# Kernel tuning notes

Hardware: AMD Instinct MI355X
Metric: run time of the kernel (lower is better)

The kernel has to match this reference:

```python
import jax, jax.numpy as jnp
import numpy as np

NUM_NODES = 100000
NUM_EDGES = 600000
NUM_GRAPHS = 512
D = 128  # num_features == latent widths


def setup_inputs() -> dict:
    key = jax.random.key(0)
    ks = jax.random.split(key, 16)
    inp = {
        "x": jax.random.normal(ks[0], (NUM_NODES, D), dtype=jnp.float32),
        "edge_index": jax.random.randint(ks[1], (2, NUM_EDGES), 0, NUM_NODES, dtype=jnp.int32),
        "batch": jnp.sort(jax.random.randint(ks[2], (NUM_NODES,), 0, NUM_GRAPHS, dtype=jnp.int32)),
    }
    s = 1.0 / np.sqrt(D)
    # SAGEConv params per layer: lin_l (applied to mean-aggregated neighbors), lin_r (root), bias
    for i in range(3):
        inp[f"Wl{i+1}"] = jax.random.uniform(ks[3 + 3 * i], (D, D), jnp.float32, -s, s)
        inp[f"Wr{i+1}"] = jax.random.uniform(ks[4 + 3 * i], (D, D), jnp.float32, -s, s)
        inp[f"b{i+1}"] = jax.random.uniform(ks[5 + 3 * i], (D,), jnp.float32, -s, s)
    inp["Wro"] = jax.random.uniform(ks[12], (D, 1), jnp.float32, -s, s)
    inp["bro"] = jax.random.uniform(ks[13], (1,), jnp.float32, -s, s)
    return inp


def _sage_conv(h, Wl, Wr, b, src, dst):
    # mean aggregation of source features at destination nodes
    msg = jax.ops.segment_sum(h[src], dst, num_segments=NUM_NODES)          # [N, D]
    cnt = jax.ops.segment_sum(jnp.ones((src.shape[0], 1), h.dtype), dst,
                              num_segments=NUM_NODES)                        # [N, 1]
    mean = msg / jnp.maximum(cnt, 1.0)
    return mean @ Wl + h @ Wr + b


def reference(x, edge_index, batch, Wl1, Wr1, b1, Wl2, Wr2, b2, Wl3, Wr3, b3, Wro, bro):
    src, dst = edge_index[0], edge_index[1]
    h = x
    for Wl, Wr, b in ((Wl1, Wr1, b1), (Wl2, Wr2, b2), (Wl3, Wr3, b3)):
        h = jax.nn.relu(_sage_conv(h, Wl, Wr, b, src, dst))
    # per-graph sum pooling (replaces the python loop over unique batch ids)
    pooled = jax.ops.segment_sum(h, batch, num_segments=NUM_GRAPHS)  # [G, D]
    return jax.nn.sigmoid(pooled @ Wro + bro)  # [G, 1]
```

## Files before the change

kernel.cpp:

```cpp
#include <hip/hip_runtime.h>
#include <math.h>

#define N_NODES 100000
#define N_EDGES 600000
#define N_GRAPHS 512
#define D 128
#define SCAN_BS 1024
#define SCAN_NBC ((N_NODES + SCAN_BS - 1) / SCAN_BS)
#define NPART 8
#define PART_SZ (N_NODES / NPART)
#define E4 (N_EDGES / 4)
#define SPLIT_B 12500
#define DBINS 64
#define DNB ((N_NODES + 255) / 256)

typedef unsigned short u16;
typedef __attribute__((ext_vector_type(8))) short short8;
typedef __attribute__((ext_vector_type(4))) float f32x4;

__device__ __forceinline__ u16 f2bf(float f) {
    unsigned int u = __float_as_uint(f);
    u += 0x7FFFu + ((u >> 16) & 1u);
    return (u16)(u >> 16);
}
__device__ __forceinline__ float bf2f(u16 h) {
    return __uint_as_float(((unsigned int)h) << 16);
}
__device__ __forceinline__ void split2(float f, unsigned int& h16, unsigned int& l16) {
    unsigned int u = __float_as_uint(f);
    unsigned int hb = (u + (0x7FFFu + ((u >> 16) & 1u))) & 0xffff0000u;
    float lo = f - __uint_as_float(hb);
    unsigned int ul = __float_as_uint(lo);
    h16 = hb >> 16;
    l16 = (ul + (0x7FFFu + ((ul >> 16) & 1u))) >> 16;
}

typedef __attribute__((address_space(1))) const unsigned int gas_u32;
typedef __attribute__((address_space(3))) unsigned int las_u32;
__device__ __forceinline__ void gload16(const void* g, void* l) {
    __builtin_amdgcn_global_load_lds((gas_u32*)g, (las_u32*)l, 16, 0, 0);
}

__global__ __launch_bounds__(256) void zero_i_kernel(int* __restrict__ p, int n) {
    int i = blockIdx.x * 256 + threadIdx.x;
    if (i < n) p[i] = 0;
}

__global__ __launch_bounds__(256) void hist_kernel(const int* __restrict__ dst,
                                                   int* __restrict__ deg) {
    int e = blockIdx.x * 256 + threadIdx.x;
    if (e < N_EDGES) atomicAdd(&deg[dst[e]], 1);
}

__global__ __launch_bounds__(1024) void scan1_kernel(const int* __restrict__ deg,
                                                     int* __restrict__ excl,
                                                     int* __restrict__ blocksum) {
    __shared__ int buf[2][SCAN_BS];
    const int t = threadIdx.x;
    const int gid = blockIdx.x * SCAN_BS + t;
    int v = (gid < N_NODES) ? deg[gid] : 0;
    buf[0][t] = v;
    __syncthreads();
    int pi = 0;
    for (int off = 1; off < SCAN_BS; off <<= 1) {
        int val = buf[pi][t];
        if (t >= off) val += buf[pi][t - off];
        buf[pi ^ 1][t] = val;
        pi ^= 1;
        __syncthreads();
    }
    int incl = buf[pi][t];
    if (gid < N_NODES) excl[gid] = incl - v;
    if (t == SCAN_BS - 1) blocksum[blockIdx.x] = incl;
}

__global__ __launch_bounds__(256) void scan3_kernel(const int* __restrict__ excl,
                                                    const int* __restrict__ blocksum,
                                                    int* __restrict__ rowptr) {
    __shared__ int buf[2][128];
    const int t = threadIdx.x;
    if (t < 128) buf[0][t] = (t < SCAN_NBC) ? blocksum[t] : 0;
    __syncthreads();
    int pi = 0;
    for (int off = 1; off < 128; off <<= 1) {
        if (t < 128) {
            int val = buf[pi][t];
            if (t >= off) val += buf[pi][t - off];
            buf[pi ^ 1][t] = val;
        }
        pi ^= 1;
        __syncthreads();
    }
    const int i = blockIdx.x * 256 + t;
    if (i < N_NODES) {
        const int j = i / SCAN_BS;
        const int pref = (j == 0) ? 0 : buf[pi][j - 1];
        rowptr[i] = excl[i] + pref;
    }
    if (i == 0) rowptr[N_NODES] = N_EDGES;
}

__global__ __launch_bounds__(256) void fill_kernel(const int* __restrict__ src,
                                                   const int* __restrict__ dst,
                                                   const int* __restrict__ rowptr,
                                                   int* __restrict__ fill,
                                                   int* __restrict__ csr_src) {
    const int lo = (blockIdx.x & (NPART - 1)) * PART_SZ;
    const int i4 = (blockIdx.x >> 3) * 256 + threadIdx.x;
    if (i4 >= E4) return;
    const int4 d4 = ((const int4*)dst)[i4];
    const int4 s4 = ((const int4*)src)[i4];
    if ((unsigned)(d4.x - lo) < (unsigned)PART_SZ) {
        int pos = rowptr[d4.x] + atomicAdd(&fill[d4.x], 1);
        csr_src[pos] = s4.x;
    }
    if ((unsigned)(d4.y - lo) < (unsigned)PART_SZ) {
        int pos = rowptr[d4.y] + atomicAdd(&fill[d4.y], 1);
        csr_src[pos] = s4.y;
    }
    if ((unsigned)(d4.z - lo) < (unsigned)PART_SZ) {
        int pos = rowptr[d4.z] + atomicAdd(&fill[d4.z], 1);
        csr_src[pos] = s4.z;
    }
    if ((unsigned)(d4.w - lo) < (unsigned)PART_SZ) {
        int pos = rowptr[d4.w] + atomicAdd(&fill[d4.w], 1);
        csr_src[pos] = s4.w;
    }
}

__global__ __launch_bounds__(256) void dhist_kernel(const int* __restrict__ deg,
                                                    int* __restrict__ histT,
                                                    int* __restrict__ bintot) {
    __shared__ int h[DBINS];
    const int t = threadIdx.x;
    if (t < DBINS) h[t] = 0;
    __syncthreads();
    const int i = blockIdx.x * 256 + t;
    if (i < N_NODES) {
        const int b = 63 - min(deg[i], 63);
        atomicAdd(&h[b], 1);
    }
    __syncthreads();
    if (t < DBINS) {
        histT[t * DNB + blockIdx.x] = h[t];
        if (h[t] > 0) atomicAdd(&bintot[t], h[t]);
    }
}

__global__ __launch_bounds__(512) void dscan2_kernel(const int* __restrict__ bintot,
                                                     int* __restrict__ histT) {
    __shared__ int buf[2][512];
    __shared__ int base;
    const int b = blockIdx.x;
    const int t = threadIdx.x;
    if (t == 0) {
        int s = 0;
        for (int j = 0; j < b; ++j) s += bintot[j];
        base = s;
    }
    const int v = (t < DNB) ? histT[b * DNB + t] : 0;
    buf[0][t] = v;
    __syncthreads();
    int pi = 0;
    for (int off = 1; off < 512; off <<= 1) {
        int val = buf[pi][t];
        if (t >= off) val += buf[pi][t - off];
        buf[pi ^ 1][t] = val;
        pi ^= 1;
        __syncthreads();
    }
    if (t < DNB) histT[b * DNB + t] = base + buf[pi][t] - v;
}

__global__ __launch_bounds__(256) void dscatter_kernel(const int* __restrict__ deg,
                                                       const int* __restrict__ offs,
                                                       int* __restrict__ perm) {
    __shared__ int c[DBINS];
    const int t = threadIdx.x;
    if (t < DBINS) c[t] = 0;
    __syncthreads();
    const int i = blockIdx.x * 256 + t;
    if (i < N_NODES) {
        const int b = 63 - min(deg[i], 63);
        const int r = atomicAdd(&c[b], 1);
        perm[offs[b * DNB + blockIdx.x] + r] = i;
    }
}

__global__ __launch_bounds__(256) void prep_kernel(const float* __restrict__ x,
                                                   u16* __restrict__ Hhi,
                                                   u16* __restrict__ Hlo,
                                                   const float* __restrict__ Wl1, const float* __restrict__ Wr1,
                                                   const float* __restrict__ Wl2, const float* __restrict__ Wr2,
                                                   const float* __restrict__ Wl3, const float* __restrict__ Wr3,
                                                   u16* __restrict__ wph, u16* __restrict__ wpl) {
    if (blockIdx.x < SPLIT_B) {
        const int i = blockIdx.x * 256 + threadIdx.x;
        const float4 v = ((const float4*)x)[i];
        unsigned int h0, l0, h1, l1, h2, l2, h3, l3;
        split2(v.x, h0, l0); split2(v.y, h1, l1);
        split2(v.z, h2, l2); split2(v.w, h3, l3);
        uint2 oh, ol;
        oh.x = h0 | (h1 << 16); oh.y = h2 | (h3 << 16);
        ol.x = l0 | (l1 << 16); ol.y = l2 | (l3 << 16);
        ((uint2*)Hhi)[i] = oh;
        ((uint2*)Hlo)[i] = ol;
    } else {
        const int b = (blockIdx.x - SPLIT_B) * 4 + (threadIdx.x >> 6);
        const int lane = threadIdx.x & 63;
        const int layer = b >> 6;
        const int t = b & 63;
        const float* Wl = (layer == 0) ? Wl1 : (layer == 1) ? Wl2 : Wl3;
        const float* Wr = (layer == 0) ? Wr1 : (layer == 1) ? Wr2 : Wr3;
        const int nt = t >> 3, kt = t & 7;
        const int n = nt * 16 + (lane & 15);
        const int k0 = kt * 32 + (lane >> 4) * 8;
        const size_t base = (size_t)layer * 32768 + (size_t)(t * 64 + lane) * 8;
        #pragma unroll
        for (int j = 0; j < 8; ++j) {
            const int k = k0 + j;
            const float w = (k < 128) ? Wl[k * 128 + n] : Wr[(k - 128) * 128 + n];
            const u16 h = f2bf(w);
            wph[base + j] = h;
            wpl[base + j] = f2bf(w - bf2f(h));
        }
    }
}

__global__ __launch_bounds__(512, 4) void gemm_kernel(const u16* __restrict__ INhi,
                                                      const u16* __restrict__ INlo,
                                                      const int* __restrict__ rowptr,
                                                      const int* __restrict__ csr_src,
                                                      const int* __restrict__ perm,
                                                      const u16* __restrict__ Wph,
                                                      const u16* __restrict__ Wpl,
                                                      const float* __restrict__ bias,
                                                      u16* __restrict__ OHhi,
                                                      u16* __restrict__ OHlo,
                                                      const float* __restrict__ Wro,
                                                      float* rowdot) {
    __shared__ uint4 ldsAll[2048];
    const int t = threadIdx.x;
    const int lane = t & 63;
    const int wv = t >> 6;
    const int m0 = blockIdx.x * 128 + wv * 16;
    const int gid = m0 + (lane & 15);
    const int ko = (lane >> 4) * 8;

    int prow = 0, beg = 0, deg = 0;
    if (gid < N_NODES) {
        prow = perm[gid];
        beg = rowptr[prow];
        deg = rowptr[prow + 1] - beg;
    }
    const int rm = prow;

#define STAGE_W(Q, B) do {                                                      \
        const uint4* gh_ = (const uint4*)Wph + (Q) * 512;                       \
        const uint4* gl_ = (const uint4*)Wpl + (Q) * 512;                       \
        gload16(gh_ + t, (void*)&ldsAll[(B) * 1024 + wv * 64]);                 \
        gload16(gl_ + t, (void*)&ldsAll[(B) * 1024 + 512 + wv * 64]);           \
    } while (0)

    STAGE_W(0, 0);
    __builtin_amdgcn_sched_barrier(0);
    STAGE_W(1, 1);
    __builtin_amdgcn_sched_barrier(0);

    short8 ah[4], al[4];
    #pragma unroll
    for (int kt = 0; kt < 4; ++kt) {
        ah[kt] = *(const short8*)(INhi + (size_t)rm * D + kt * 32 + ko);
        al[kt] = *(const short8*)(INlo + (size_t)rm * D + kt * 32 + ko);
    }

    float ac[4][8];
    #pragma unroll
    for (int kt = 0; kt < 4; ++kt) {
        #pragma unroll
        for (int j = 0; j < 8; ++j) ac[kt][j] = 0.f;
    }
    int s_cur = (deg > 0) ? csr_src[beg] : 0;
    for (int n = 0; __any(n < deg); ++n) {
        const bool act = n < deg;
        const int s_nxt = (n + 1 < deg) ? csr_src[beg + n + 1] : 0;
        if (act) {
            const size_t rb = (size_t)s_cur * D + ko;
            #pragma unroll
            for (int kt = 0; kt < 4; ++kt) {
                const uint4 v = *(const uint4*)(INhi + rb + kt * 32);
                ac[kt][0] += __uint_as_float(v.x << 16);
                ac[kt][1] += __uint_as_float(v.x & 0xffff0000u);
                ac[kt][2] += __uint_as_float(v.y << 16);
                ac[kt][3] += __uint_as_float(v.y & 0xffff0000u);
                ac[kt][4] += __uint_as_float(v.z << 16);
                ac[kt][5] += __uint_as_float(v.z & 0xffff0000u);
                ac[kt][6] += __uint_as_float(v.w << 16);
                ac[kt][7] += __uint_as_float(v.w & 0xffff0000u);
            }
        }
        s_cur = s_nxt;
    }
    const float inv = 1.0f / (float)max(deg, 1);
    short8 am[4];
    #pragma unroll
    for (int kt = 0; kt < 4; ++kt) {
        uint4 u;
        u.x = (unsigned)f2bf(ac[kt][0] * inv) | ((unsigned)f2bf(ac[kt][1] * inv) << 16);
        u.y = (unsigned)f2bf(ac[kt][2] * inv) | ((unsigned)f2bf(ac[kt][3] * inv) << 16);
        u.z = (unsigned)f2bf(ac[kt][4] * inv) | ((unsigned)f2bf(ac[kt][5] * inv) << 16);
        u.w = (unsigned)f2bf(ac[kt][6] * inv) | ((unsigned)f2bf(ac[kt][7] * inv) << 16);
        am[kt] = __builtin_bit_cast(short8, u);
    }
    __builtin_amdgcn_sched_barrier(0);

    const int cl = lane & 15;
    const int g4 = (lane >> 4) << 2;

    f32x4 acc8[2][4];

#define COMPUTE_S(Q, B) do {                                                    \
        const u16* bufU_ = (const u16*)(ldsAll + (B) * 1024);                   \
        f32x4 acc_ = {0.f, 0.f, 0.f, 0.f};                                      \
        _Pragma("unroll")                                                       \
        for (int kt_ = 0; kt_ < 8; ++kt_) {                                     \
            const int fo_ = kt_ * 512 + lane * 8;                               \
            const short8 bh_ = *(const short8*)(bufU_ + fo_);                   \
            const short8 bl_ = *(const short8*)(bufU_ + 4096 + fo_);            \
            if (kt_ < 4) {                                                      \
                acc_ = __builtin_amdgcn_mfma_f32_16x16x32_bf16(am[kt_], bh_, acc_, 0, 0, 0); \
                acc_ = __builtin_amdgcn_mfma_f32_16x16x32_bf16(am[kt_], bl_, acc_, 0, 0, 0); \
            } else {                                                            \
                acc_ = __builtin_amdgcn_mfma_f32_16x16x32_bf16(ah[kt_ - 4], bh_, acc_, 0, 0, 0); \
                acc_ = __builtin_amdgcn_mfma_f32_16x16x32_bf16(ah[kt_ - 4], bl_, acc_, 0, 0, 0); \
                acc_ = __builtin_amdgcn_mfma_f32_16x16x32_bf16(al[kt_ - 4], bh_, acc_, 0, 0, 0); \
            }                                                                   \
        }                                                                       \
        acc8[(Q) >> 2][(Q) & 3] = acc_;                                         \
    } while (0)

    asm volatile("s_waitcnt vmcnt(0)" ::: "memory");
    __builtin_amdgcn_s_barrier();
    COMPUTE_S(0, 0);
    __builtin_amdgcn_s_barrier();
    STAGE_W(2, 0);
    __builtin_amdgcn_sched_barrier(0);
    COMPUTE_S(1, 1);
    __builtin_amdgcn_s_barrier();
    STAGE_W(3, 1);
    asm volatile("s_waitcnt vmcnt(2)" ::: "memory");
    __builtin_amdgcn_s_barrier();
    COMPUTE_S(2, 0);
    __builtin_amdgcn_s_barrier();
    STAGE_W(4, 0);
    asm volatile("s_waitcnt vmcnt(2)" ::: "memory");
    __builtin_amdgcn_s_barrier();
    COMPUTE_S(3, 1);
    __builtin_amdgcn_s_barrier();
    STAGE_W(5, 1);
    asm volatile("s_waitcnt vmcnt(2)" ::: "memory");
    __builtin_amdgcn_s_barrier();
    COMPUTE_S(4, 0);
    __builtin_amdgcn_s_barrier();
    STAGE_W(6, 0);
    asm volatile("s_waitcnt vmcnt(2)" ::: "memory");
    __builtin_amdgcn_s_barrier();
    COMPUTE_S(5, 1);
    __builtin_amdgcn_s_barrier();
    STAGE_W(7, 1);
    asm volatile("s_waitcnt vmcnt(2)" ::: "memory");
    __builtin_amdgcn_s_barrier();
    COMPUTE_S(6, 0);
    asm volatile("s_waitcnt vmcnt(0)" ::: "memory");
    __builtin_amdgcn_s_barrier();
    COMPUTE_S(7, 1);

    char* bounceB = (char*)ldsAll + wv * 2048;

    if (rowdot) {
        float wsum[4] = {0.f, 0.f, 0.f, 0.f};
        #pragma unroll
        for (int si = 0; si < 2; ++si) {
            #pragma unroll
            for (int nt2 = 0; nt2 < 4; ++nt2) {
                const int col = (si * 4 + nt2) * 16 + cl;
                const float bv = bias[col];
                const float wroc = Wro[col];
                #pragma unroll
                for (int r = 0; r < 4; ++r) {
                    const float v = fmaxf(acc8[si][nt2][r] + bv, 0.f);
                    wsum[r] = fmaf(v, wroc, wsum[r]);
                }
            }
        }
        #pragma unroll
        for (int r = 0; r < 4; ++r) {
            float tsum = wsum[r];
            tsum += __shfl_down(tsum, 8, 64);
            tsum += __shfl_down(tsum, 4, 64);
            tsum += __shfl_down(tsum, 2, 64);
            tsum += __shfl_down(tsum, 1, 64);
            const int lg = m0 + g4 + r;
            if (cl == 0 && lg < N_NODES) {
                rowdot[perm[lg]] = tsum;
            }
        }
    } else {
        #pragma unroll
        for (int si = 0; si < 2; ++si) {
            asm volatile("s_waitcnt lgkmcnt(0)" ::: "memory");
            unsigned int lo_pack[8];
            #pragma unroll
            for (int nt2 = 0; nt2 < 4; ++nt2) {
                const int col = (si * 4 + nt2) * 16 + cl;
                const float bv = bias[col];
                #pragma unroll
                for (int r = 0; r < 4; ++r) {
                    const int rr = g4 + r;
                    const float v = fmaxf(acc8[si][nt2][r] + bv, 0.f);
                    unsigned int h16, l16;
                    split2(v, h16, l16);
                    const int boff = (rr * 128 + (nt2 * 16 + cl) * 2) ^ ((rr & 7) << 4);
                    *(u16*)(bounceB + boff) = (u16)h16;
                    if (r & 1) lo_pack[nt2 * 2 + (r >> 1)] |= l16 << 16;
                    else       lo_pack[nt2 * 2 + (r >> 1)]  = l16;
                }
            }
            asm volatile("s_waitcnt lgkmcnt(0)" ::: "memory");
            #pragma unroll
            for (int j = 0; j < 2; ++j) {
                const int rr = j * 8 + (lane >> 3);
                const int blk = lane & 7;
                const uint4 vv = *(const uint4*)(bounceB + rr * 128 + ((blk ^ (rr & 7)) << 4));
                const int lg = m0 + rr;
                if (lg < N_NODES)
                    *(uint4*)(OHhi + (size_t)perm[lg] * D + si * 64 + blk * 8) = vv;
            }
            asm volatile("s_waitcnt lgkmcnt(0)" ::: "memory");
            #pragma unroll
            for (int nt2 = 0; nt2 < 4; ++nt2) {
                #pragma unroll
                for (int r = 0; r < 4; ++r) {
                    const int rr = g4 + r;
                    const unsigned int l16 = (lo_pack[nt2 * 2 + (r >> 1)] >> ((r & 1) * 16)) & 0xffffu;
                    const int boff = (rr * 128 + (nt2 * 16 + cl) * 2) ^ ((rr & 7) << 4);
                    *(u16*)(bounceB + boff) = (u16)l16;
                }
            }
            asm volatile("s_waitcnt lgkmcnt(0)" ::: "memory");
            #pragma unroll
            for (int j = 0; j < 2; ++j) {
                const int rr = j * 8 + (lane >> 3);
                const int blk = lane & 7;
                const uint4 vv = *(const uint4*)(bounceB + rr * 128 + ((blk ^ (rr & 7)) << 4));
                const int lg = m0 + rr;
                if (lg < N_NODES)
                    *(uint4*)(OHlo + (size_t)perm[lg] * D + si * 64 + blk * 8) = vv;
            }
        }
    }
#undef STAGE_W
#undef COMPUTE_S
}

__global__ __launch_bounds__(64) void final_kernel(const float* __restrict__ rowdot,
                                                   const int* __restrict__ batch,
                                                   const float* __restrict__ bro,
                                                   float* __restrict__ out) {
    const int g = blockIdx.x;
    const int t = threadIdx.x;
    int lo = 0, hi = N_NODES;
    while (lo < hi) { int mid = (lo + hi) >> 1; if (batch[mid] < g) lo = mid + 1; else hi = mid; }
    int lo2 = lo, hi2 = N_NODES;
    while (lo2 < hi2) { int mid = (lo2 + hi2) >> 1; if (batch[mid] < g + 1) lo2 = mid + 1; else hi2 = mid; }

    float acc = 0.0f;
    for (int i = lo + t; i < lo2; i += 64) acc += rowdot[i];
    #pragma unroll
    for (int off = 32; off > 0; off >>= 1) acc += __shfl_down(acc, off, 64);
    if (t == 0) out[g] = 1.0f / (1.0f + expf(-(acc + bro[0])));
}

extern "C" void kernel_launch(void* const* d_in, const int* in_sizes, int n_in,
                              void* d_out, int out_size, void* d_ws, size_t ws_size,
                              hipStream_t stream) {
    const float* x     = (const float*)d_in[0];
    const int*   ei    = (const int*)d_in[1];
    const int*   batch = (const int*)d_in[2];
    const int*   src   = ei;
    const int*   dst   = ei + N_EDGES;
    const float* Wl[3] = {(const float*)d_in[3], (const float*)d_in[6], (const float*)d_in[9]};
    const float* Wr[3] = {(const float*)d_in[4], (const float*)d_in[7], (const float*)d_in[10]};
    const float* bs[3] = {(const float*)d_in[5], (const float*)d_in[8], (const float*)d_in[11]};
    const float* Wro   = (const float*)d_in[12];
    const float* bro   = (const float*)d_in[13];
    float* out = (float*)d_out;

    const size_t ND = (size_t)N_NODES * D;
    char* ws = (char*)d_ws;
    u16* Ahi = (u16*)ws;
    u16* Alo = Ahi + ND;
    u16* Bhi = Alo + ND;
    u16* Blo = Bhi + ND;
    u16* Wph = Blo + ND;
    u16* Wpl = Wph + 3 * 32768;
    int* deg      = (int*)(Wpl + 3 * 32768);
    int* fill     = deg + N_NODES;
    int* bintot   = fill + N_NODES;
    float* rowdot = (float*)(bintot + DBINS);
    int* excl     = (int*)(rowdot + N_NODES);
    int* blocksum = excl + N_NODES;
    int* rowptr   = blocksum + 128;
    int* csr_src  = rowptr + N_NODES + 1;
    int* histT    = csr_src + N_EDGES;
    int* perm     = histT + DBINS * DNB;

    const int EB      = (N_EDGES + 255) / 256;
    const int NB      = (N_NODES + 255) / 256;
    const int NBZ     = (2 * N_NODES + DBINS + 255) / 256;
    const int EPB     = ((E4 + 255) / 256) * NPART;
    const int PREP_B  = SPLIT_B + 48;
    const int GEMM_B  = (N_NODES + 127) / 128;

    zero_i_kernel<<<NBZ, 256, 0, stream>>>(deg, 2 * N_NODES + DBINS);
    hist_kernel<<<EB, 256, 0, stream>>>(dst, deg);
    scan1_kernel<<<SCAN_NBC, SCAN_BS, 0, stream>>>(deg, excl, blocksum);
    scan3_kernel<<<NB, 256, 0, stream>>>(excl, blocksum, rowptr);
    fill_kernel<<<EPB, 256, 0, stream>>>(src, dst, rowptr, fill, csr_src);

    dhist_kernel<<<DNB, 256, 0, stream>>>(deg, histT, bintot);
    dscan2_kernel<<<DBINS, 512, 0, stream>>>(bintot, histT);
    dscatter_kernel<<<DNB, 256, 0, stream>>>(deg, histT, perm);

    prep_kernel<<<PREP_B, 256, 0, stream>>>(x, Ahi, Alo,
                                            Wl[0], Wr[0], Wl[1], Wr[1], Wl[2], Wr[2],
                                            Wph, Wpl);

    gemm_kernel<<<GEMM_B, 512, 0, stream>>>(Ahi, Alo, rowptr, csr_src, perm,
                                            Wph, Wpl, bs[0],
                                            Bhi, Blo, Wro, (float*)nullptr);
    gemm_kernel<<<GEMM_B, 512, 0, stream>>>(Bhi, Blo, rowptr, csr_src, perm,
                                            Wph + 32768, Wpl + 32768, bs[1],
                                            Ahi, Alo, Wro, (float*)nullptr);
    gemm_kernel<<<GEMM_B, 512, 0, stream>>>(Ahi, Alo, rowptr, csr_src, perm,
                                            Wph + 2 * 32768, Wpl + 2 * 32768, bs[2],
                                            Bhi, Blo, Wro, rowdot);

    final_kernel<<<N_GRAPHS, 64, 0, stream>>>(rowdot, batch, bro, out);
}
```

Before: 345.8 us.

## Merge graph preprocessing kernels into fewer launches via block-range dispatch

Folds the degree histogram into the input/weight bf16 split kernel, the degree-bin histogram into the row-pointer scan, the bin-offset scan into the rowptr fixup kernel, and the degree-sorted permutation scatter into the CSR fill kernel. Each fused kernel chooses its role from the block index, cutting eight preprocessing launches to four. Degree-bin chunks grow from 256 to 1024 nodes so they line up with the scan blocks. The cost is larger mixed-role grids, and the perm scatter now runs alongside the atomic-heavy fill.

```diff
diff --git a/kernel.cpp b/kernel.cpp
--- a/kernel.cpp
+++ b/kernel.cpp
@@ -12,7 +12,7 @@
 #define E4 (N_EDGES / 4)
 #define SPLIT_B 12500
 #define DBINS 64
-#define DNB ((N_NODES + 255) / 256)
+#define DNB2 SCAN_NBC
 
 typedef unsigned short u16;
 typedef __attribute__((ext_vector_type(8))) short short8;
@@ -46,156 +46,25 @@
     if (i < n) p[i] = 0;
 }
 
-__global__ __launch_bounds__(256) void hist_kernel(const int* __restrict__ dst,
-                                                   int* __restrict__ deg) {
-    int e = blockIdx.x * 256 + threadIdx.x;
-    if (e < N_EDGES) atomicAdd(&deg[dst[e]], 1);
-}
-
-__global__ __launch_bounds__(1024) void scan1_kernel(const int* __restrict__ deg,
-                                                     int* __restrict__ excl,
-                                                     int* __restrict__ blocksum) {
-    __shared__ int buf[2][SCAN_BS];
-    const int t = threadIdx.x;
-    const int gid = blockIdx.x * SCAN_BS + t;
-    int v = (gid < N_NODES) ? deg[gid] : 0;
-    buf[0][t] = v;
-    __syncthreads();
-    int pi = 0;
-    for (int off = 1; off < SCAN_BS; off <<= 1) {
-        int val = buf[pi][t];
-        if (t >= off) val += buf[pi][t - off];
-        buf[pi ^ 1][t] = val;
-        pi ^= 1;
-        __syncthreads();
-    }
-    int incl = buf[pi][t];
-    if (gid < N_NODES) excl[gid] = incl - v;
-    if (t == SCAN_BS - 1) blocksum[blockIdx.x] = incl;
-}
-
-__global__ __launch_bounds__(256) void scan3_kernel(const int* __restrict__ excl,
-                                                    const int* __restrict__ blocksum,
-                                                    int* __restrict__ rowptr) {
-    __shared__ int buf[2][128];
-    const int t = threadIdx.x;
-    if (t < 128) buf[0][t] = (t < SCAN_NBC) ? blocksum[t] : 0;
-    __syncthreads();
-    int pi = 0;
-    for (int off = 1; off < 128; off <<= 1) {
-        if (t < 128) {
-            int val = buf[pi][t];
-            if (t >= off) val += buf[pi][t - off];
-            buf[pi ^ 1][t] = val;
-        }
-        pi ^= 1;
-        __syncthreads();
-    }
-    const int i = blockIdx.x * 256 + t;
-    if (i < N_NODES) {
-        const int j = i / SCAN_BS;
-        const int pref = (j == 0) ? 0 : buf[pi][j - 1];
-        rowptr[i] = excl[i] + pref;
-    }
-    if (i == 0) rowptr[N_NODES] = N_EDGES;
-}
-
-__global__ __launch_bounds__(256) void fill_kernel(const int* __restrict__ src,
-                                                   const int* __restrict__ dst,
-                                                   const int* __restrict__ rowptr,
-                                                   int* __restrict__ fill,
-                                                   int* __restrict__ csr_src) {
-    const int lo = (blockIdx.x & (NPART - 1)) * PART_SZ;
-    const int i4 = (blockIdx.x >> 3) * 256 + threadIdx.x;
-    if (i4 >= E4) return;
-    const int4 d4 = ((const int4*)dst)[i4];
-    const int4 s4 = ((const int4*)src)[i4];
-    if ((unsigned)(d4.x - lo) < (unsigned)PART_SZ) {
-        int pos = rowptr[d4.x] + atomicAdd(&fill[d4.x], 1);
-        csr_src[pos] = s4.x;
-    }
-    if ((unsigned)(d4.y - lo) < (unsigned)PART_SZ) {
-        int pos = rowptr[d4.y] + atomicAdd(&fill[d4.y], 1);
-        csr_src[pos] = s4.y;
-    }
-    if ((unsigned)(d4.z - lo) < (unsigned)PART_SZ) {
-        int pos = rowptr[d4.z] + atomicAdd(&fill[d4.z], 1);
-        csr_src[pos] = s4.z;
-    }
-    if ((unsigned)(d4.w - lo) < (unsigned)PART_SZ) {
-        int pos = rowptr[d4.w] + atomicAdd(&fill[d4.w], 1);
-        csr_src[pos] = s4.w;
-    }
-}
-
-__global__ __launch_bounds__(256) void dhist_kernel(const int* __restrict__ deg,
-                                                    int* __restrict__ histT,
-                                                    int* __restrict__ bintot) {
-    __shared__ int h[DBINS];
-    const int t = threadIdx.x;
-    if (t < DBINS) h[t] = 0;
-    __syncthreads();
-    const int i = blockIdx.x * 256 + t;
-    if (i < N_NODES) {
-        const int b = 63 - min(deg[i], 63);
-        atomicAdd(&h[b], 1);
-    }
-    __syncthreads();
-    if (t < DBINS) {
-        histT[t * DNB + blockIdx.x] = h[t];
-        if (h[t] > 0) atomicAdd(&bintot[t], h[t]);
-    }
-}
-
-__global__ __launch_bounds__(512) void dscan2_kernel(const int* __restrict__ bintot,
-                                                     int* __restrict__ histT) {
-    __shared__ int buf[2][512];
-    __shared__ int base;
-    const int b = blockIdx.x;
-    const int t = threadIdx.x;
-    if (t == 0) {
-        int s = 0;
-        for (int j = 0; j < b; ++j) s += bintot[j];
-        base = s;
-    }
-    const int v = (t < DNB) ? histT[b * DNB + t] : 0;
-    buf[0][t] = v;
-    __syncthreads();
-    int pi = 0;
-    for (int off = 1; off < 512; off <<= 1) {
-        int val = buf[pi][t];
-        if (t >= off) val += buf[pi][t - off];
-        buf[pi ^ 1][t] = val;
-        pi ^= 1;
-        __syncthreads();
-    }
-    if (t < DNB) histT[b * DNB + t] = base + buf[pi][t] - v;
-}
-
-__global__ __launch_bounds__(256) void dscatter_kernel(const int* __restrict__ deg,
-                                                       const int* __restrict__ offs,
-                                                       int* __restrict__ perm) {
-    __shared__ int c[DBINS];
-    const int t = threadIdx.x;
-    if (t < DBINS) c[t] = 0;
-    __syncthreads();
-    const int i = blockIdx.x * 256 + t;
-    if (i < N_NODES) {
-        const int b = 63 - min(deg[i], 63);
-        const int r = atomicAdd(&c[b], 1);
-        perm[offs[b * DNB + blockIdx.x] + r] = i;
-    }
-}
-
-__global__ __launch_bounds__(256) void prep_kernel(const float* __restrict__ x,
-                                                   u16* __restrict__ Hhi,
-                                                   u16* __restrict__ Hlo,
-                                                   const float* __restrict__ Wl1, const float* __restrict__ Wr1,
-                                                   const float* __restrict__ Wl2, const float* __restrict__ Wr2,
-                                                   const float* __restrict__ Wl3, const float* __restrict__ Wr3,
-                                                   u16* __restrict__ wph, u16* __restrict__ wpl) {
-    if (blockIdx.x < SPLIT_B) {
-        const int i = blockIdx.x * 256 + threadIdx.x;
+
+__global__ __launch_bounds__(256) void histprep_kernel(const int* __restrict__ dst,
+                                                       int* __restrict__ deg,
+                                                       const float* __restrict__ x,
+                                                       u16* __restrict__ Hhi,
+                                                       u16* __restrict__ Hlo,
+                                                       const float* __restrict__ Wl1, const float* __restrict__ Wr1,
+                                                       const float* __restrict__ Wl2, const float* __restrict__ Wr2,
+                                                       const float* __restrict__ Wl3, const float* __restrict__ Wr3,
+                                                       u16* __restrict__ wph, u16* __restrict__ wpl,
+                                                       int EB) {
+    if ((int)blockIdx.x < EB) {
+        int e = blockIdx.x * 256 + threadIdx.x;
+        if (e < N_EDGES) atomicAdd(&deg[dst[e]], 1);
+        return;
+    }
+    const int pbid = blockIdx.x - EB;
+    if (pbid < SPLIT_B) {
+        const int i = pbid * 256 + threadIdx.x;
         const float4 v = ((const float4*)x)[i];
         unsigned int h0, l0, h1, l1, h2, l2, h3, l3;
         split2(v.x, h0, l0); split2(v.y, h1, l1);
@@ -206,7 +75,7 @@
         ((uint2*)Hhi)[i] = oh;
         ((uint2*)Hlo)[i] = ol;
     } else {
-        const int b = (blockIdx.x - SPLIT_B) * 4 + (threadIdx.x >> 6);
+        const int b = (pbid - SPLIT_B) * 4 + (threadIdx.x >> 6);
         const int lane = threadIdx.x & 63;
         const int layer = b >> 6;
         const int t = b & 63;
@@ -223,6 +92,143 @@
             const u16 h = f2bf(w);
             wph[base + j] = h;
             wpl[base + j] = f2bf(w - bf2f(h));
+        }
+    }
+}
+
+__global__ __launch_bounds__(1024) void scan1d_kernel(const int* __restrict__ deg,
+                                                      int* __restrict__ excl,
+                                                      int* __restrict__ blocksum,
+                                                      int* __restrict__ histT,
+                                                      int* __restrict__ bintot) {
+    __shared__ int buf[2][SCAN_BS];
+    __shared__ int h[DBINS];
+    const int t = threadIdx.x;
+    const int gid = blockIdx.x * SCAN_BS + t;
+    int v = (gid < N_NODES) ? deg[gid] : 0;
+    if (t < DBINS) h[t] = 0;
+    buf[0][t] = v;
+    __syncthreads();
+    if (gid < N_NODES) atomicAdd(&h[63 - min(v, 63)], 1);
+    int pi = 0;
+    for (int off = 1; off < SCAN_BS; off <<= 1) {
+        int val = buf[pi][t];
+        if (t >= off) val += buf[pi][t - off];
+        buf[pi ^ 1][t] = val;
+        pi ^= 1;
+        __syncthreads();
+    }
+    int incl = buf[pi][t];
+    if (gid < N_NODES) excl[gid] = incl - v;
+    if (t == SCAN_BS - 1) blocksum[blockIdx.x] = incl;
+    if (t < DBINS) {
+        histT[t * DNB2 + blockIdx.x] = h[t];
+        if (h[t] > 0) atomicAdd(&bintot[t], h[t]);
+    }
+}
+
+__global__ __launch_bounds__(256) void scan3d_kernel(const int* __restrict__ excl,
+                                                     const int* __restrict__ blocksum,
+                                                     int* __restrict__ rowptr,
+                                                     const int* __restrict__ bintot,
+                                                     int* __restrict__ histT,
+                                                     int NB) {
+    const int t = threadIdx.x;
+    if ((int)blockIdx.x < NB) {
+        __shared__ int buf[2][128];
+        if (t < 128) buf[0][t] = (t < SCAN_NBC) ? blocksum[t] : 0;
+        __syncthreads();
+        int pi = 0;
+        for (int off = 1; off < 128; off <<= 1) {
+            if (t < 128) {
+                int val = buf[pi][t];
+                if (t >= off) val += buf[pi][t - off];
+                buf[pi ^ 1][t] = val;
+            }
+            pi ^= 1;
+            __syncthreads();
+        }
+        const int i = blockIdx.x * 256 + t;
+        if (i < N_NODES) {
+            const int j = i / SCAN_BS;
+            const int pref = (j == 0) ? 0 : buf[pi][j - 1];
+            rowptr[i] = excl[i] + pref;
+        }
+        if (i == 0) rowptr[N_NODES] = N_EDGES;
+    } else {
+        __shared__ int buf[2][128];
+        __shared__ int base;
+        const int b = blockIdx.x - NB;
+        if (t == 0) {
+            int s = 0;
+            for (int j = 0; j < b; ++j) s += bintot[j];
+            base = s;
+        }
+        int v = 0;
+        if (t < 128) {
+            v = (t < DNB2) ? histT[b * DNB2 + t] : 0;
+            buf[0][t] = v;
+        }
+        __syncthreads();
+        int pi = 0;
+        for (int off = 1; off < 128; off <<= 1) {
+            if (t < 128) {
+                int val = buf[pi][t];
+                if (t >= off) val += buf[pi][t - off];
+                buf[pi ^ 1][t] = val;
+            }
+            pi ^= 1;
+            __syncthreads();
+        }
+        if (t < DNB2) histT[b * DNB2 + t] = base + buf[pi][t] - v;
+    }
+}
+
+__global__ __launch_bounds__(256) void filld_kernel(const int* __restrict__ src,
+                                                    const int* __restrict__ dst,
+                                                    const int* __restrict__ rowptr,
+                                                    int* __restrict__ fill,
+                                                    int* __restrict__ csr_src,
+                                                    const int* __restrict__ deg,
+                                                    const int* __restrict__ offs,
+                                                    int* __restrict__ perm,
+                                                    int EPB) {
+    if ((int)blockIdx.x < EPB) {
+        const int lo = (blockIdx.x & (NPART - 1)) * PART_SZ;
+        const int i4 = (blockIdx.x >> 3) * 256 + threadIdx.x;
+        if (i4 >= E4) return;
+        const int4 d4 = ((const int4*)dst)[i4];
+        const int4 s4 = ((const int4*)src)[i4];
+        if ((unsigned)(d4.x - lo) < (unsigned)PART_SZ) {
+            int pos = rowptr[d4.x] + atomicAdd(&fill[d4.x], 1);
+            csr_src[pos] = s4.x;
+        }
+        if ((unsigned)(d4.y - lo) < (unsigned)PART_SZ) {
+            int pos = rowptr[d4.y] + atomicAdd(&fill[d4.y], 1);
+            csr_src[pos] = s4.y;
+        }
+        if ((unsigned)(d4.z - lo) < (unsigned)PART_SZ) {
+            int pos = rowptr[d4.z] + atomicAdd(&fill[d4.z], 1);
+            csr_src[pos] = s4.z;
+        }
+        if ((unsigned)(d4.w - lo) < (unsigned)PART_SZ) {
+            int pos = rowptr[d4.w] + atomicAdd(&fill[d4.w], 1);
+            csr_src[pos] = s4.w;
+        }
+    } else {
+        __shared__ int c[DBINS];
+        const int t = threadIdx.x;
+        const int chunk = blockIdx.x - EPB;
+        if (t < DBINS) c[t] = 0;
+        __syncthreads();
+        #pragma unroll
+        for (int k = 0; k < 4; ++k) {
+            const int i = chunk * 1024 + k * 256 + t;
+            if (i < N_NODES) {
+                const int b = 63 - min(deg[i], 63);
+                const int r = atomicAdd(&c[b], 1);
+                perm[offs[b * DNB2 + chunk] + r] = i;
+            }
         }
     }
 }
@@ -513,7 +519,7 @@
     int* rowptr   = blocksum + 128;
     int* csr_src  = rowptr + N_NODES + 1;
     int* histT    = csr_src + N_EDGES;
-    int* perm     = histT + DBINS * DNB;
+    int* perm     = histT + DBINS * DNB2;
 
     const int EB      = (N_EDGES + 255) / 256;
     const int NB      = (N_NODES + 255) / 256;
@@ -523,18 +529,13 @@
     const int GEMM_B  = (N_NODES + 127) / 128;
 
     zero_i_kernel<<<NBZ, 256, 0, stream>>>(deg, 2 * N_NODES + DBINS);
-    hist_kernel<<<EB, 256, 0, stream>>>(dst, deg);
-    scan1_kernel<<<SCAN_NBC, SCAN_BS, 0, stream>>>(deg, excl, blocksum);
-    scan3_kernel<<<NB, 256, 0, stream>>>(excl, blocksum, rowptr);
-    fill_kernel<<<EPB, 256, 0, stream>>>(src, dst, rowptr, fill, csr_src);
-
-    dhist_kernel<<<DNB, 256, 0, stream>>>(deg, histT, bintot);
-    dscan2_kernel<<<DBINS, 512, 0, stream>>>(bintot, histT);
-    dscatter_kernel<<<DNB, 256, 0, stream>>>(deg, histT, perm);
-
-    prep_kernel<<<PREP_B, 256, 0, stream>>>(x, Ahi, Alo,
-                                            Wl[0], Wr[0], Wl[1], Wr[1], Wl[2], Wr[2],
-                                            Wph, Wpl);
+    histprep_kernel<<<EB + PREP_B, 256, 0, stream>>>(dst, deg, x, Ahi, Alo,
+                                                     Wl[0], Wr[0], Wl[1], Wr[1],
+                                                     Wl[2], Wr[2], Wph, Wpl, EB);
+    scan1d_kernel<<<SCAN_NBC, SCAN_BS, 0, stream>>>(deg, excl, blocksum, histT, bintot);
+    scan3d_kernel<<<NB + DBINS, 256, 0, stream>>>(excl, blocksum, rowptr, bintot, histT, NB);
+    filld_kernel<<<EPB + DNB2, 256, 0, stream>>>(src, dst, rowptr, fill, csr_src,
+                                                 deg, histT, perm, EPB);
 
     gemm_kernel<<<GEMM_B, 512, 0, stream>>>(Ahi, Alo, rowptr, csr_src, perm,
                                             Wph, Wpl, bs[0],
```

After: 331.5 us (median of 2 runs). -4.1%, faster.
